# Optimization experiments

Hardware: AMD Instinct MI355X
Metric: run time of the kernel (lower is better)

The kernel has to match this reference:

```python
import jax, jax.numpy as jnp
import numpy as np
from math import sqrt

D_MODEL = 1024
N_HEADS = 16
E = D_MODEL // N_HEADS  # d_keys = d_values = 64


def setup_inputs() -> dict:
    key = jax.random.key(0)
    ks = jax.random.split(key, 11)
    B, L, S = 2, 2048, 2048
    s = 1.0 / sqrt(D_MODEL)
    return {
        "queries": jax.random.normal(ks[0], (B, L, D_MODEL), jnp.float32),
        "keys": jax.random.normal(ks[1], (B, S, D_MODEL), jnp.float32),
        "values": jax.random.normal(ks[2], (B, S, D_MODEL), jnp.float32),
        "Wq": jax.random.normal(ks[3], (D_MODEL, D_MODEL), jnp.float32) * s,
        "bq": jnp.zeros((D_MODEL,), jnp.float32),
        "Wk": jax.random.normal(ks[4], (D_MODEL, D_MODEL), jnp.float32) * s,
        "bk": jnp.zeros((D_MODEL,), jnp.float32),
        "Wv": jax.random.normal(ks[5], (D_MODEL, D_MODEL), jnp.float32) * s,
        "bv": jnp.zeros((D_MODEL,), jnp.float32),
        "Wo": jax.random.normal(ks[6], (D_MODEL, D_MODEL), jnp.float32) * s,
        "bo": jnp.zeros((D_MODEL,), jnp.float32),
    }


def reference(queries, keys, values, Wq, bq, Wk, bk, Wv, bv, Wo, bo):
    B, L, _ = queries.shape
    S = keys.shape[1]
    H = N_HEADS
    # projections -> [B, L/S, H, E]
    q = (queries @ Wq + bq).reshape(B, L, H, E)
    k = (keys @ Wk + bk).reshape(B, S, H, E)
    v = (values @ Wv + bv).reshape(B, S, H, E)
    scale = 1.0 / sqrt(E)
    scores = jnp.einsum('blhe,bshe->bhls', q, k)  # [B,H,L,S]
    A = jax.nn.softmax(scale * scores, axis=-1)   # dropout = identity (eval)
    V = jnp.einsum('bhls,bshd->blhd', A, v)       # [B,L,H,E]
    out = V.reshape(B, L, H * E) @ Wo + bo
    return out
```

## Files before the change

kernel.cpp:

```cpp
#include <hip/hip_runtime.h>
#include <hip/hip_bf16.h>
#include <stdint.h>

#define BATCH 2
#define SEQ   2048
#define DM    1024
#define NH    16
#define EH    64
#define MROWS (BATCH*SEQ)

typedef __attribute__((ext_vector_type(8))) short  short8;
typedef __attribute__((ext_vector_type(4))) float  floatx4;
typedef __attribute__((ext_vector_type(8))) unsigned short ushort8v;
typedef __attribute__((ext_vector_type(4))) unsigned short ushort4v;

__device__ __forceinline__ unsigned short f2bf(float f) {
    return (unsigned short)((__float_as_uint(f) + 0x8000u) >> 16);
}

__device__ __forceinline__ void gload_lds16(const void* g, void* l) {
    __builtin_amdgcn_global_load_lds(
        (const __attribute__((address_space(1))) unsigned int*)g,
        (__attribute__((address_space(3))) unsigned int*)l, 16, 0, 0);
}

__global__ __launch_bounds__(256)
void transpose_w(const float* __restrict__ W0, const float* __restrict__ W1,
                 const float* __restrict__ W2, const float* __restrict__ W3,
                 unsigned short* __restrict__ T0, unsigned short* __restrict__ T1,
                 unsigned short* __restrict__ T2, unsigned short* __restrict__ T3,
                 int zbase)
{
    int z = zbase + blockIdx.z;
    const float* W = (z == 0) ? W0 : (z == 1) ? W1 : (z == 2) ? W2 : W3;
    unsigned short* T = (z == 0) ? T0 : (z == 1) ? T1 : (z == 2) ? T2 : T3;
    __shared__ float t[32][33];
    const int tid = threadIdx.x;
    const int k0 = blockIdx.y * 32, n0 = blockIdx.x * 32;
    {
        int r = tid >> 3, c4 = (tid & 7) * 4;
        float4 u = *(const float4*)&W[(size_t)(k0 + r) * DM + n0 + c4];
        t[r][c4 + 0] = u.x; t[r][c4 + 1] = u.y; t[r][c4 + 2] = u.z; t[r][c4 + 3] = u.w;
    }
    __syncthreads();
    {
        int n = tid >> 3, k4 = (tid & 7) * 4;
        ushort4v o;
        o[0] = f2bf(t[k4 + 0][n]); o[1] = f2bf(t[k4 + 1][n]);
        o[2] = f2bf(t[k4 + 2][n]); o[3] = f2bf(t[k4 + 3][n]);
        *(ushort4v*)&T[(size_t)(n0 + n) * DM + k0 + k4] = o;
    }
}

struct GemmArgs {
    const void* A[3];
    const unsigned short* W[3];
    const float* bias[3];
    void* C[3];
    int   outmode[3];
    float oscale[3];
};

template<int AMODE, int NT>
__global__ __launch_bounds__(256)
void gemm_mfma(GemmArgs ga)
{
    constexpr int BN = NT * 16;
    const int z = blockIdx.z;
    const void* Ag = ga.A[z];
    const unsigned short* Wt = ga.W[z];
    void* Cg = ga.C[z];

    __shared__ unsigned short As[128 * 32];
    __shared__ unsigned short Bs[BN * 32];

    const int tid = threadIdx.x;
    const int lane = tid & 63, w = tid >> 6;
    const int lane15 = lane & 15, quad = lane >> 4;
    const int row0 = blockIdx.y * 128, col0 = blockIdx.x * BN;

    floatx4 acc[2][NT] = {};

    for (int kt = 0; kt < DM; kt += 32) {
        __syncthreads();
        if (AMODE == 1) {
            const unsigned short* A = (const unsigned short*)Ag;
#pragma unroll
            for (int rr = 0; rr < 2; ++rr) {
                int c = rr * 256 + w * 64 + lane;
                int row = c >> 2, kel = (c & 3) * 8;
                gload_lds16(&A[(size_t)(row0 + row) * DM + kt + kel],
                            (char*)As + (size_t)(rr * 256 + w * 64) * 16);
            }
        } else {
            const float* A = (const float*)Ag;
#pragma unroll
            for (int rr = 0; rr < 2; ++rr) {
                int c = rr * 256 + tid;
                int row = c >> 2, kel = (c & 3) * 8;
                const float* p = &A[(size_t)(row0 + row) * DM + kt + kel];
                float4 u0 = *(const float4*)p;
                float4 u1 = *(const float4*)(p + 4);
                ushort8v o8;
                o8[0] = f2bf(u0.x); o8[1] = f2bf(u0.y); o8[2] = f2bf(u0.z); o8[3] = f2bf(u0.w);
                o8[4] = f2bf(u1.x); o8[5] = f2bf(u1.y); o8[6] = f2bf(u1.z); o8[7] = f2bf(u1.w);
                *(ushort8v*)&As[(size_t)c * 8] = o8;
            }
        }
        {
#pragma unroll
            for (int rr = 0; rr < BN / 64; ++rr) {
                int c = rr * 256 + w * 64 + lane;
                int row = c >> 2, kel = (c & 3) * 8;
                gload_lds16(&Wt[(size_t)(col0 + row) * DM + kt + kel],
                            (char*)Bs + (size_t)(rr * 256 + w * 64) * 16);
            }
        }
        __syncthreads();

        short8 af[2], bf[NT];
#pragma unroll
        for (int i = 0; i < 2; ++i)
            af[i] = *(const short8*)&As[(w * 32 + i * 16 + lane15) * 32 + quad * 8];
#pragma unroll
        for (int j = 0; j < NT; ++j)
            bf[j] = *(const short8*)&Bs[(j * 16 + lane15) * 32 + quad * 8];
#pragma unroll
        for (int i = 0; i < 2; ++i)
#pragma unroll
            for (int j = 0; j < NT; ++j)
                acc[i][j] = __builtin_amdgcn_mfma_f32_16x16x32_bf16(af[i], bf[j], acc[i][j], 0, 0, 0);
    }

    const float* bias = ga.bias[z];
    const int om = ga.outmode[z];
    const float os = ga.oscale[z];
#pragma unroll
    for (int i = 0; i < 2; ++i) {
#pragma unroll
        for (int j = 0; j < NT; ++j) {
#pragma unroll
            for (int r = 0; r < 4; ++r) {
                int row = row0 + w * 32 + i * 16 + quad * 4 + r;
                int col = col0 + j * 16 + lane15;
                float v = (acc[i][j][r] + bias[col]) * os;
                if (om == 0) {
                    ((float*)Cg)[(size_t)row * DM + col] = v;
                } else {
                    int b = row >> 11, l = row & (SEQ - 1);
                    int h = col >> 6, e = col & (EH - 1);
                    size_t o = ((size_t)(b * NH + h) * SEQ + l) * EH + e;
                    ((unsigned short*)Cg)[o] = f2bf(v);
                }
            }
        }
    }
}

__global__ __launch_bounds__(256)
void gemm_vT(const unsigned short* __restrict__ WvT,
             const float* __restrict__ vals,
             const float* __restrict__ bv,
             unsigned short* __restrict__ Vt)
{
    __shared__ unsigned short As[128 * 32];
    __shared__ unsigned short Bs[128 * 32];

    const int tid = threadIdx.x;
    const int lane = tid & 63, w = tid >> 6;
    const int lane15 = lane & 15, quad = lane >> 4;
    const int row0 = blockIdx.y * 128;
    const int col0 = blockIdx.x * 128;

    floatx4 acc[2][8] = {};

    for (int kt = 0; kt < DM; kt += 32) {
        __syncthreads();
#pragma unroll
        for (int rr = 0; rr < 2; ++rr) {
            int c = rr * 256 + w * 64 + lane;
            int row = c >> 2, kel = (c & 3) * 8;
            gload_lds16(&WvT[(size_t)(row0 + row) * DM + kt + kel],
                        (char*)As + (size_t)(rr * 256 + w * 64) * 16);
        }
#pragma unroll
        for (int rr = 0; rr < 2; ++rr) {
            int c = rr * 256 + tid;
            int row = c >> 2, kel = (c & 3) * 8;
            const float* p = &vals[(size_t)(col0 + row) * DM + kt + kel];
            float4 u0 = *(const float4*)p;
            float4 u1 = *(const float4*)(p + 4);
            ushort8v o8;
            o8[0] = f2bf(u0.x); o8[1] = f2bf(u0.y); o8[2] = f2bf(u0.z); o8[3] = f2bf(u0.w);
            o8[4] = f2bf(u1.x); o8[5] = f2bf(u1.y); o8[6] = f2bf(u1.z); o8[7] = f2bf(u1.w);
            *(ushort8v*)&Bs[(size_t)c * 8] = o8;
        }
        __syncthreads();

        short8 af[2], bf[8];
#pragma unroll
        for (int i = 0; i < 2; ++i)
            af[i] = *(const short8*)&As[(w * 32 + i * 16 + lane15) * 32 + quad * 8];
#pragma unroll
        for (int j = 0; j < 8; ++j)
            bf[j] = *(const short8*)&Bs[(j * 16 + lane15) * 32 + quad * 8];
#pragma unroll
        for (int i = 0; i < 2; ++i)
#pragma unroll
            for (int j = 0; j < 8; ++j)
                acc[i][j] = __builtin_amdgcn_mfma_f32_16x16x32_bf16(af[i], bf[j], acc[i][j], 0, 0, 0);
    }

#pragma unroll
    for (int i = 0; i < 2; ++i) {
#pragma unroll
        for (int j = 0; j < 8; ++j) {
#pragma unroll
            for (int r = 0; r < 4; ++r) {
                int row = row0 + w * 32 + i * 16 + quad * 4 + r;
                int col = col0 + j * 16 + lane15;
                float v = acc[i][j][r] + bv[row];
                int h = row >> 6, e = row & (EH - 1);
                int b = col >> 11, l = col & (SEQ - 1);
                Vt[((size_t)(b * NH + h) * EH + e) * SEQ + l] = f2bf(v);
            }
        }
    }
}

__device__ __forceinline__ void stage_kv(const unsigned short* __restrict__ Kp,
                                         const unsigned short* __restrict__ Vp,
                                         int st, unsigned short* ksb, unsigned short* vsb,
                                         int w, int lane)
{
#pragma unroll
    for (int rr = 0; rr < 2; ++rr) {
        int p = rr * 256 + w * 64 + lane;
        int row = p >> 3;
        int gch = (p & 7) ^ (row & 7);
        gload_lds16(&Kp[(size_t)(st + row) * EH + gch * 8],
                    ksb + (size_t)(rr * 256 + w * 64) * 8);
        gload_lds16(&Vp[(size_t)row * SEQ + st + gch * 8],
                    vsb + (size_t)(rr * 256 + w * 64) * 8);
    }
}

__global__ __launch_bounds__(256)
void attn_mfma(const unsigned short* __restrict__ Qh,
               const unsigned short* __restrict__ Kh,
               const unsigned short* __restrict__ Vt,
               unsigned short* __restrict__ ctx)
{
    __shared__ unsigned short Ks[2][64 * 64];
    __shared__ unsigned short Vs[2][64 * 64];
    __shared__ unsigned short Ps[128][72];

    const int tid = threadIdx.x;
    const int lane = tid & 63, w = tid >> 6;
    const int lane15 = lane & 15, quad = lane >> 4;
    const int qt = blockIdx.x, h = blockIdx.y, b = blockIdx.z;
    const size_t bh = (size_t)(b * NH + h);
    const unsigned short* Kp = Kh + bh * SEQ * EH;
    const unsigned short* Vp = Vt + bh * EH * SEQ;

    short8 qf[2][2];
    {
        const unsigned short* Qp =
            Qh + (bh * SEQ + (size_t)qt * 128 + w * 32 + lane15) * EH;
#pragma unroll
        for (int ks = 0; ks < 2; ++ks) {
            qf[0][ks] = *(const short8*)(Qp + ks * 32 + quad * 8);
            qf[1][ks] = *(const short8*)(Qp + 16 * EH + ks * 32 + quad * 8);
        }
    }
    short8 ones;
#pragma unroll
    for (int i = 0; i < 8; ++i) ones[i] = (short)0x3F80;

    floatx4 o[2][4] = {};
    floatx4 lacc[2] = {};

    stage_kv(Kp, Vp, 0, Ks[0], Vs[0], w, lane);
    __syncthreads();
    int cur = 0;

    for (int st = 0; st < SEQ; st += 64) {
        int nxt = cur ^ 1;
        if (st + 64 < SEQ)
            stage_kv(Kp, Vp, st + 64, Ks[nxt], Vs[nxt], w, lane);
        const unsigned short* ksb = Ks[cur];
        const unsigned short* vsb = Vs[cur];

        floatx4 sacc[4][2] = {};
#pragma unroll
        for (int ts = 0; ts < 4; ++ts) {
#pragma unroll
            for (int ks = 0; ks < 2; ++ks) {
                short8 kf = *(const short8*)&ksb[((ts * 16 + lane15) << 6) +
                                                 ((((ks << 2) + quad) ^ (lane15 & 7)) << 3)];
                sacc[ts][0] = __builtin_amdgcn_mfma_f32_16x16x32_bf16(kf, qf[0][ks], sacc[ts][0], 0, 0, 0);
                sacc[ts][1] = __builtin_amdgcn_mfma_f32_16x16x32_bf16(kf, qf[1][ks], sacc[ts][1], 0, 0, 0);
            }
        }

#pragma unroll
        for (int ts = 0; ts < 4; ++ts)
#pragma unroll
            for (int nq = 0; nq < 2; ++nq) {
                unsigned int u0 = __float_as_uint(__builtin_amdgcn_exp2f(sacc[ts][nq][0])) + 0x8000u;
                unsigned int u1 = __float_as_uint(__builtin_amdgcn_exp2f(sacc[ts][nq][1])) + 0x8000u;
                unsigned int u2 = __float_as_uint(__builtin_amdgcn_exp2f(sacc[ts][nq][2])) + 0x8000u;
                unsigned int u3 = __float_as_uint(__builtin_amdgcn_exp2f(sacc[ts][nq][3])) + 0x8000u;
                uint2 pk;
                pk.x = (u0 >> 16) | (u1 & 0xFFFF0000u);
                pk.y = (u2 >> 16) | (u3 & 0xFFFF0000u);
                *(uint2*)&Ps[w * 32 + nq * 16 + lane15][ts * 16 + quad * 4] = pk;
            }

#pragma unroll
        for (int ks = 0; ks < 2; ++ks) {
            short8 pf[2];
#pragma unroll
            for (int mt = 0; mt < 2; ++mt) {
                pf[mt] = *(const short8*)&Ps[w * 32 + mt * 16 + lane15][ks * 32 + quad * 8];
                lacc[mt] = __builtin_amdgcn_mfma_f32_16x16x32_bf16(pf[mt], ones, lacc[mt], 0, 0, 0);
            }
#pragma unroll
            for (int t2 = 0; t2 < 4; ++t2) {
                short8 vf = *(const short8*)&vsb[((t2 * 16 + lane15) << 6) +
                                                 ((((ks << 2) + quad) ^ (lane15 & 7)) << 3)];
                o[0][t2] = __builtin_amdgcn_mfma_f32_16x16x32_bf16(pf[0], vf, o[0][t2], 0, 0, 0);
                o[1][t2] = __builtin_amdgcn_mfma_f32_16x16x32_bf16(pf[1], vf, o[1][t2], 0, 0, 0);
            }
        }
        __syncthreads();
        cur = nxt;
    }

#pragma unroll
    for (int mt = 0; mt < 2; ++mt) {
        float inv[4];
#pragma unroll
        for (int r = 0; r < 4; ++r) inv[r] = 1.0f / lacc[mt][r];
#pragma unroll
        for (int t2 = 0; t2 < 4; ++t2)
#pragma unroll
            for (int r = 0; r < 4; ++r) {
                int q = qt * 128 + w * 32 + mt * 16 + quad * 4 + r;
                int col = h * EH + t2 * 16 + lane15;
                ctx[((size_t)(b * SEQ + q)) * DM + col] = f2bf(o[mt][t2][r] * inv[r]);
            }
    }
}

extern "C" void kernel_launch(void* const* d_in, const int* in_sizes, int n_in,
                              void* d_out, int out_size, void* d_ws, size_t ws_size,
                              hipStream_t stream)
{
    const float* queries = (const float*)d_in[0];
    const float* keys    = (const float*)d_in[1];
    const float* values  = (const float*)d_in[2];
    const float* Wq = (const float*)d_in[3];
    const float* bq = (const float*)d_in[4];
    const float* Wk = (const float*)d_in[5];
    const float* bk = (const float*)d_in[6];
    const float* Wv = (const float*)d_in[7];
    const float* bv = (const float*)d_in[8];
    const float* Wo = (const float*)d_in[9];
    const float* bo = (const float*)d_in[10];
    float* out = (float*)d_out;

    unsigned short* ws = (unsigned short*)d_ws;
    const size_t MAT = (size_t)MROWS * DM;
    const size_t WSZ = (size_t)DM * DM;
    unsigned short* Qhp = ws;
    unsigned short* Khp = ws + MAT;
    unsigned short* Vtp = ws + 2 * MAT;
    unsigned short* ctx = ws + 3 * MAT;
    unsigned short* WqT = ctx;
    unsigned short* WkT = ctx + WSZ;
    unsigned short* WvT = ctx + 2 * WSZ;
    unsigned short* WoT = ws;

    const float qscale = 0.125f * 1.44269504088896f;

    transpose_w<<<dim3(DM / 32, DM / 32, 3), 256, 0, stream>>>(
        Wq, Wk, Wv, Wo, WqT, WkT, WvT, WoT, 0);

    GemmArgs pa;
    pa.A[0] = queries; pa.A[1] = keys;  pa.A[2] = keys;
    pa.W[0] = WqT;     pa.W[1] = WkT;   pa.W[2] = WkT;
    pa.bias[0] = bq;   pa.bias[1] = bk; pa.bias[2] = bk;
    pa.C[0] = Qhp;     pa.C[1] = Khp;   pa.C[2] = Khp;
    pa.outmode[0] = 1; pa.outmode[1] = 1; pa.outmode[2] = 1;
    pa.oscale[0] = qscale; pa.oscale[1] = 1.f; pa.oscale[2] = 1.f;
    gemm_mfma<0, 8><<<dim3(8, 32, 2), 256, 0, stream>>>(pa);

    gemm_vT<<<dim3(32, 8), 256, 0, stream>>>(WvT, values, bv, Vtp);

    attn_mfma<<<dim3(SEQ / 128, NH, BATCH), 256, 0, stream>>>(Qhp, Khp, Vtp, ctx);

    transpose_w<<<dim3(DM / 32, DM / 32, 1), 256, 0, stream>>>(
        Wq, Wk, Wv, Wo, WqT, WkT, WvT, WoT, 3);

    GemmArgs oa;
    oa.A[0] = ctx; oa.W[0] = WoT; oa.bias[0] = bo; oa.C[0] = out;
    oa.outmode[0] = 0; oa.oscale[0] = 1.f;
    oa.A[1] = oa.A[0]; oa.W[1] = oa.W[0]; oa.bias[1] = oa.bias[0]; oa.C[1] = oa.C[0];
    oa.outmode[1] = 0; oa.oscale[1] = 1.f;
    oa.A[2] = oa.A[0]; oa.W[2] = oa.W[0]; oa.bias[2] = oa.bias[0]; oa.C[2] = oa.C[0];
    oa.outmode[2] = 0; oa.oscale[2] = 1.f;
    gemm_mfma<1, 4><<<dim3(16, 32, 1), 256, 0, stream>>>(oa);
}
```

Measured before the change: 278.0 us.

## Fuse Q/K/V projections into one launch with column-major block swizzle

Merges the V-transposed projection into the same kernel launch as the Q and K projections, using blockIdx.z=2 to take the transposed path. The launch count drops by one, and three projections now fill the device at once instead of two plus a separate smaller launch. Block indices are remapped so consecutive blocks share weight or activation tiles, which should improve L2 reuse. The output GEMM gets its own specialized kernel with the same rasterization, replacing the templated generic kernel with its runtime outmode branch.

```diff
diff --git a/kernel.cpp b/kernel.cpp
--- a/kernel.cpp
+++ b/kernel.cpp
@@ -52,53 +52,45 @@
     }
 }
 
-struct GemmArgs {
-    const void* A[3];
-    const unsigned short* W[3];
+struct ProjArgs {
+    const float* act[3];
+    const unsigned short* wt[3];
     const float* bias[3];
-    void* C[3];
-    int   outmode[3];
+    unsigned short* C[3];
     float oscale[3];
 };
 
-template<int AMODE, int NT>
 __global__ __launch_bounds__(256)
-void gemm_mfma(GemmArgs ga)
-{
-    constexpr int BN = NT * 16;
+void proj_qkv(ProjArgs pa)
+{
     const int z = blockIdx.z;
-    const void* Ag = ga.A[z];
-    const unsigned short* Wt = ga.W[z];
-    void* Cg = ga.C[z];
+    const bool vt = (z == 2);
+    const int linear = (int)(blockIdx.x + gridDim.x * blockIdx.y);
+    int rb, cb;
+    if (!vt) { rb = linear & 31; cb = linear >> 5; }
+    else     { cb = linear & 31; rb = linear >> 5; }
+    const int row0 = rb * 128, col0 = cb * 128;
+
+    const float* act = pa.act[z];
+    const unsigned short* wt = pa.wt[z];
 
     __shared__ unsigned short As[128 * 32];
-    __shared__ unsigned short Bs[BN * 32];
+    __shared__ unsigned short Bs[128 * 32];
 
     const int tid = threadIdx.x;
     const int lane = tid & 63, w = tid >> 6;
     const int lane15 = lane & 15, quad = lane >> 4;
-    const int row0 = blockIdx.y * 128, col0 = blockIdx.x * BN;
-
-    floatx4 acc[2][NT] = {};
+
+    floatx4 acc[2][8] = {};
 
     for (int kt = 0; kt < DM; kt += 32) {
         __syncthreads();
-        if (AMODE == 1) {
-            const unsigned short* A = (const unsigned short*)Ag;
-#pragma unroll
-            for (int rr = 0; rr < 2; ++rr) {
-                int c = rr * 256 + w * 64 + lane;
-                int row = c >> 2, kel = (c & 3) * 8;
-                gload_lds16(&A[(size_t)(row0 + row) * DM + kt + kel],
-                            (char*)As + (size_t)(rr * 256 + w * 64) * 16);
-            }
-        } else {
-            const float* A = (const float*)Ag;
+        if (!vt) {
 #pragma unroll
             for (int rr = 0; rr < 2; ++rr) {
                 int c = rr * 256 + tid;
                 int row = c >> 2, kel = (c & 3) * 8;
-                const float* p = &A[(size_t)(row0 + row) * DM + kt + kel];
+                const float* p = &act[(size_t)(row0 + row) * DM + kt + kel];
                 float4 u0 = *(const float4*)p;
                 float4 u1 = *(const float4*)(p + 4);
                 ushort8v o8;
@@ -106,51 +98,71 @@
                 o8[4] = f2bf(u1.x); o8[5] = f2bf(u1.y); o8[6] = f2bf(u1.z); o8[7] = f2bf(u1.w);
                 *(ushort8v*)&As[(size_t)c * 8] = o8;
             }
-        }
-        {
-#pragma unroll
-            for (int rr = 0; rr < BN / 64; ++rr) {
+#pragma unroll
+            for (int rr = 0; rr < 2; ++rr) {
                 int c = rr * 256 + w * 64 + lane;
                 int row = c >> 2, kel = (c & 3) * 8;
-                gload_lds16(&Wt[(size_t)(col0 + row) * DM + kt + kel],
+                gload_lds16(&wt[(size_t)(col0 + row) * DM + kt + kel],
                             (char*)Bs + (size_t)(rr * 256 + w * 64) * 16);
             }
+        } else {
+#pragma unroll
+            for (int rr = 0; rr < 2; ++rr) {
+                int c = rr * 256 + w * 64 + lane;
+                int row = c >> 2, kel = (c & 3) * 8;
+                gload_lds16(&wt[(size_t)(row0 + row) * DM + kt + kel],
+                            (char*)As + (size_t)(rr * 256 + w * 64) * 16);
+            }
+#pragma unroll
+            for (int rr = 0; rr < 2; ++rr) {
+                int c = rr * 256 + tid;
+                int row = c >> 2, kel = (c & 3) * 8;
+                const float* p = &act[(size_t)(col0 + row) * DM + kt + kel];
+                float4 u0 = *(const float4*)p;
+                float4 u1 = *(const float4*)(p + 4);
+                ushort8v o8;
+                o8[0] = f2bf(u0.x); o8[1] = f2bf(u0.y); o8[2] = f2bf(u0.z); o8[3] = f2bf(u0.w);
+                o8[4] = f2bf(u1.x); o8[5] = f2bf(u1.y); o8[6] = f2bf(u1.z); o8[7] = f2bf(u1.w);
+                *(ushort8v*)&Bs[(size_t)c * 8] = o8;
+            }
         }
         __syncthreads();
 
-        short8 af[2], bf[NT];
+        short8 af[2], bf[8];
 #pragma unroll
         for (int i = 0; i < 2; ++i)
             af[i] = *(const short8*)&As[(w * 32 + i * 16 + lane15) * 32 + quad * 8];
 #pragma unroll
-        for (int j = 0; j < NT; ++j)
+        for (int j = 0; j < 8; ++j)
             bf[j] = *(const short8*)&Bs[(j * 16 + lane15) * 32 + quad * 8];
 #pragma unroll
         for (int i = 0; i < 2; ++i)
 #pragma unroll
-            for (int j = 0; j < NT; ++j)
+            for (int j = 0; j < 8; ++j)
                 acc[i][j] = __builtin_amdgcn_mfma_f32_16x16x32_bf16(af[i], bf[j], acc[i][j], 0, 0, 0);
     }
 
-    const float* bias = ga.bias[z];
-    const int om = ga.outmode[z];
-    const float os = ga.oscale[z];
+    const float* bias = pa.bias[z];
+    const float os = pa.oscale[z];
+    unsigned short* C = pa.C[z];
 #pragma unroll
     for (int i = 0; i < 2; ++i) {
 #pragma unroll
-        for (int j = 0; j < NT; ++j) {
+        for (int j = 0; j < 8; ++j) {
 #pragma unroll
             for (int r = 0; r < 4; ++r) {
                 int row = row0 + w * 32 + i * 16 + quad * 4 + r;
                 int col = col0 + j * 16 + lane15;
-                float v = (acc[i][j][r] + bias[col]) * os;
-                if (om == 0) {
-                    ((float*)Cg)[(size_t)row * DM + col] = v;
+                if (!vt) {
+                    float v = (acc[i][j][r] + bias[col]) * os;
+                    int b = row >> 11, l = row & (SEQ - 1);
+                    int h = col >> 6,  e = col & (EH - 1);
+                    C[((size_t)(b * NH + h) * SEQ + l) * EH + e] = f2bf(v);
                 } else {
-                    int b = row >> 11, l = row & (SEQ - 1);
-                    int h = col >> 6, e = col & (EH - 1);
-                    size_t o = ((size_t)(b * NH + h) * SEQ + l) * EH + e;
-                    ((unsigned short*)Cg)[o] = f2bf(v);
+                    float v = acc[i][j][r] + bias[row];
+                    int h = row >> 6,  e = row & (EH - 1);
+                    int b = col >> 11, l = col & (SEQ - 1);
+                    C[((size_t)(b * NH + h) * EH + e) * SEQ + l] = f2bf(v);
                 }
             }
         }
@@ -158,21 +170,23 @@
 }
 
 __global__ __launch_bounds__(256)
-void gemm_vT(const unsigned short* __restrict__ WvT,
-             const float* __restrict__ vals,
-             const float* __restrict__ bv,
-             unsigned short* __restrict__ Vt)
-{
+void gemm_out(const unsigned short* __restrict__ ctx,
+              const unsigned short* __restrict__ WoT,
+              const float* __restrict__ bo,
+              float* __restrict__ out)
+{
+    const int linear = (int)(blockIdx.x + gridDim.x * blockIdx.y);
+    const int rb = linear & 31, cb = linear >> 5;
+    const int row0 = rb * 128, col0 = cb * 64;
+
     __shared__ unsigned short As[128 * 32];
-    __shared__ unsigned short Bs[128 * 32];
+    __shared__ unsigned short Bs[64 * 32];
 
     const int tid = threadIdx.x;
     const int lane = tid & 63, w = tid >> 6;
     const int lane15 = lane & 15, quad = lane >> 4;
-    const int row0 = blockIdx.y * 128;
-    const int col0 = blockIdx.x * 128;
-
-    floatx4 acc[2][8] = {};
+
+    floatx4 acc[2][4] = {};
 
     for (int kt = 0; kt < DM; kt += 32) {
         __syncthreads();
@@ -180,52 +194,41 @@
         for (int rr = 0; rr < 2; ++rr) {
             int c = rr * 256 + w * 64 + lane;
             int row = c >> 2, kel = (c & 3) * 8;
-            gload_lds16(&WvT[(size_t)(row0 + row) * DM + kt + kel],
+            gload_lds16(&ctx[(size_t)(row0 + row) * DM + kt + kel],
                         (char*)As + (size_t)(rr * 256 + w * 64) * 16);
         }
-#pragma unroll
-        for (int rr = 0; rr < 2; ++rr) {
-            int c = rr * 256 + tid;
+        {
+            int c = w * 64 + lane;
             int row = c >> 2, kel = (c & 3) * 8;
-            const float* p = &vals[(size_t)(col0 + row) * DM + kt + kel];
-            float4 u0 = *(const float4*)p;
-            float4 u1 = *(const float4*)(p + 4);
-            ushort8v o8;
-            o8[0] = f2bf(u0.x); o8[1] = f2bf(u0.y); o8[2] = f2bf(u0.z); o8[3] = f2bf(u0.w);
-            o8[4] = f2bf(u1.x); o8[5] = f2bf(u1.y); o8[6] = f2bf(u1.z); o8[7] = f2bf(u1.w);
-            *(ushort8v*)&Bs[(size_t)c * 8] = o8;
+            gload_lds16(&WoT[(size_t)(col0 + row) * DM + kt + kel],
+                        (char*)Bs + (size_t)(w * 64) * 16);
         }
         __syncthreads();
 
-        short8 af[2], bf[8];
+        short8 af[2], bf[4];
 #pragma unroll
         for (int i = 0; i < 2; ++i)
             af[i] = *(const short8*)&As[(w * 32 + i * 16 + lane15) * 32 + quad * 8];
 #pragma unroll
-        for (int j = 0; j < 8; ++j)
+        for (int j = 0; j < 4; ++j)
             bf[j] = *(const short8*)&Bs[(j * 16 + lane15) * 32 + quad * 8];
 #pragma unroll
         for (int i = 0; i < 2; ++i)
 #pragma unroll
-            for (int j = 0; j < 8; ++j)
+            for (int j = 0; j < 4; ++j)
                 acc[i][j] = __builtin_amdgcn_mfma_f32_16x16x32_bf16(af[i], bf[j], acc[i][j], 0, 0, 0);
     }
 
 #pragma unroll
-    for (int i = 0; i < 2; ++i) {
-#pragma unroll
-        for (int j = 0; j < 8; ++j) {
+    for (int i = 0; i < 2; ++i)
+#pragma unroll
+        for (int j = 0; j < 4; ++j)
 #pragma unroll
             for (int r = 0; r < 4; ++r) {
                 int row = row0 + w * 32 + i * 16 + quad * 4 + r;
                 int col = col0 + j * 16 + lane15;
-                float v = acc[i][j][r] + bv[row];
-                int h = row >> 6, e = row & (EH - 1);
-                int b = col >> 11, l = col & (SEQ - 1);
-                Vt[((size_t)(b * NH + h) * EH + e) * SEQ + l] = f2bf(v);
-            }
-        }
-    }
+                out[(size_t)row * DM + col] = acc[i][j][r] + bo[col];
+            }
 }
 
 __device__ __forceinline__ void stage_kv(const unsigned short* __restrict__ Kp,
@@ -387,28 +390,18 @@
     transpose_w<<<dim3(DM / 32, DM / 32, 3), 256, 0, stream>>>(
         Wq, Wk, Wv, Wo, WqT, WkT, WvT, WoT, 0);
 
-    GemmArgs pa;
-    pa.A[0] = queries; pa.A[1] = keys;  pa.A[2] = keys;
-    pa.W[0] = WqT;     pa.W[1] = WkT;   pa.W[2] = WkT;
-    pa.bias[0] = bq;   pa.bias[1] = bk; pa.bias[2] = bk;
-    pa.C[0] = Qhp;     pa.C[1] = Khp;   pa.C[2] = Khp;
-    pa.outmode[0] = 1; pa.outmode[1] = 1; pa.outmode[2] = 1;
+    ProjArgs pa;
+    pa.act[0] = queries; pa.act[1] = keys; pa.act[2] = values;
+    pa.wt[0] = WqT;      pa.wt[1] = WkT;   pa.wt[2] = WvT;
+    pa.bias[0] = bq;     pa.bias[1] = bk;  pa.bias[2] = bv;
+    pa.C[0] = Qhp;       pa.C[1] = Khp;    pa.C[2] = Vtp;
     pa.oscale[0] = qscale; pa.oscale[1] = 1.f; pa.oscale[2] = 1.f;
-    gemm_mfma<0, 8><<<dim3(8, 32, 2), 256, 0, stream>>>(pa);
-
-    gemm_vT<<<dim3(32, 8), 256, 0, stream>>>(WvT, values, bv, Vtp);
+    proj_qkv<<<dim3(8, 32, 3), 256, 0, stream>>>(pa);
 
     attn_mfma<<<dim3(SEQ / 128, NH, BATCH), 256, 0, stream>>>(Qhp, Khp, Vtp, ctx);
 
     transpose_w<<<dim3(DM / 32, DM / 32, 1), 256, 0, stream>>>(
         Wq, Wk, Wv, Wo, WqT, WkT, WvT, WoT, 3);
 
-    GemmArgs oa;
-    oa.A[0] = ctx; oa.W[0] = WoT; oa.bias[0] = bo; oa.C[0] = out;
-    oa.outmode[0] = 0; oa.oscale[0] = 1.f;
-    oa.A[1] = oa.A[0]; oa.W[1] = oa.W[0]; oa.bias[1] = oa.bias[0]; oa.C[1] = oa.C[0];
-    oa.outmode[1] = 0; oa.oscale[1] = 1.f;
-    oa.A[2] = oa.A[0]; oa.W[2] = oa.W[0]; oa.bias[2] = oa.bias[0]; oa.C[2] = oa.C[0];
-    oa.outmode[2] = 0; oa.oscale[2] = 1.f;
-    gemm_mfma<1, 4><<<dim3(16, 32, 1), 256, 0, stream>>>(oa);
-}
+    gemm_out<<<dim3(16, 32), 256, 0, stream>>>(ctx, WoT, bo, out);
+}
```

Measured after the change: 245.5 us. -11.7%, faster.
